# Optimization experiments

Measured on AMD Instinct MI355X. Metric: run time of the kernel, lower is better.

The kernel has to match this reference:

```python
import jax, jax.numpy as jnp
import numpy as np

NEG_INF = -1e9

def setup_inputs() -> dict:
    key = jax.random.key(0)
    ks = jax.random.split(key, 7)
    B, NQ, NK, DQ, DK, DV, DH = 16, 128, 2048, 256, 256, 128, 64
    queries = jax.random.normal(ks[0], (B, NQ, DQ), dtype=jnp.float32)
    keys = jax.random.normal(ks[1], (B, NK, DK), dtype=jnp.float32)
    values = jax.random.normal(ks[2], (B, NK, DV), dtype=jnp.float32)
    valid_lens = jax.random.randint(ks[3], (B,), 1, NK + 1, dtype=jnp.int32)
    Wq = jax.random.normal(ks[4], (DQ, DH), dtype=jnp.float32) / np.sqrt(DQ)
    Wk = jax.random.normal(ks[5], (DK, DH), dtype=jnp.float32) / np.sqrt(DK)
    wv = jax.random.normal(ks[6], (DH,), dtype=jnp.float32) / np.sqrt(DH)
    return {"queries": queries, "keys": keys, "values": values,
            "valid_lens": valid_lens, "Wq": Wq, "Wk": Wk, "wv": wv}


def reference(queries, keys, values, valid_lens, Wq, Wk, wv):
    # Additive (Bahdanau) attention.
    q = jnp.einsum('bqd,dh->bqh', queries, Wq)   # [B, nq, dH]
    k = jnp.einsum('bkd,dh->bkh', keys, Wk)      # [B, nk, dH]
    # broadcast add -> tanh -> reduce with wv: scores [B, nq, nk]
    feat = jnp.tanh(q[:, :, None, :] + k[:, None, :, :])  # [B, nq, nk, dH]
    scores = jnp.einsum('bqkh,h->bqk', feat, wv)
    # masked softmax over nk using per-batch valid lengths
    nk = keys.shape[1]
    mask = jnp.arange(nk)[None, None, :] < valid_lens[:, None, None]  # [B,1,nk]
    scores = jnp.where(mask, scores, NEG_INF)
    attn = jax.nn.softmax(scores, axis=-1)
    # dropout is identity at eval time
    return jnp.einsum('bqk,bkv->bqv', attn, values)  # [B, nq, dv]
```

## Files before the change

kernel.cpp:

```cpp
#include <hip/hip_runtime.h>
#include <stddef.h>


__device__ __forceinline__ float fast_rcp(float x)  { return __builtin_amdgcn_rcpf(x); }
__device__ __forceinline__ float fast_exp2(float x) { return __builtin_amdgcn_exp2f(x); }

#define C2F 2.88539008177792681f
#define L2E 1.44269504088896340f

#if __has_builtin(__builtin_amdgcn_global_load_lds)
#define HAS_GLL 1
__device__ __forceinline__ void gload_lds16(const void* gsrc, void* ldst) {
  __builtin_amdgcn_global_load_lds(
      (const __attribute__((address_space(1))) unsigned int*)gsrc,
      (__attribute__((address_space(3))) unsigned int*)ldst, 16, 0, 0);
}
#else
#define HAS_GLL 0
#endif

#define M_CNTS 0
#define M_NS   1
#define M_PSC  32

template<int MODE>
__device__ __forceinline__
void proj_body(const float* __restrict__ inb, const float* __restrict__ W,
               float* __restrict__ out, const float* __restrict__ wv,
               int b, int r0, int rowsPerB, int t)
{
  __shared__ float4 Wlds[256 * 16];
  __shared__ float  klds[64 * 36];

  const float4* W4 = (const float4*)W;
#if HAS_GLL
  {
    float4* wdst = Wlds + (t & ~63);
    #pragma unroll
    for (int i = 0; i < 16; ++i)
      gload_lds16(W4 + t + 256 * i, wdst + 256 * i);
  }
#else
  #pragma unroll
  for (int i = 0; i < 16; ++i) Wlds[t + 256 * i] = W4[t + 256 * i];
#endif

  const int j = t >> 4;
  const int g = t & 15;

  float acc[4][4];
  #pragma unroll
  for (int m = 0; m < 4; ++m)
    acc[m][0] = acc[m][1] = acc[m][2] = acc[m][3] = 0.f;

  for (int dc = 0; dc < 8; ++dc) {
    {
      const int row = t >> 2, cs = (t & 3) * 8;
      const float* s = inb + row * 256 + dc * 32 + cs;
      float4 a0 = *(const float4*)s;
      float4 a1 = *(const float4*)(s + 4);
      float* dst = &klds[row * 36 + cs];
      *(float4*)dst       = a0;
      *(float4*)(dst + 4) = a1;
    }
    __syncthreads();
    #pragma unroll
    for (int d4 = 0; d4 < 8; ++d4) {
      float4 kv4[4];
      #pragma unroll
      for (int m = 0; m < 4; ++m)
        kv4[m] = *(const float4*)&klds[(g + 16 * m) * 36 + d4 * 4];
      #pragma unroll
      for (int dd = 0; dd < 4; ++dd) {
        float4 w4 = Wlds[(dc * 32 + d4 * 4 + dd) * 16 + j];
        #pragma unroll
        for (int m = 0; m < 4; ++m) {
          float kv = ((const float*)&kv4[m])[dd];
          acc[m][0] = fmaf(kv, w4.x, acc[m][0]);
          acc[m][1] = fmaf(kv, w4.y, acc[m][1]);
          acc[m][2] = fmaf(kv, w4.z, acc[m][2]);
          acc[m][3] = fmaf(kv, w4.w, acc[m][3]);
        }
      }
    }
    __syncthreads();
  }

  if constexpr (MODE == 1) {
    #pragma unroll
    for (int m = 0; m < 4; ++m) {
      int k = r0 + g + 16 * m;
      size_t base = ((size_t)(b * 16 + (k >> 7)) * 64) * 128 + (k & 127);
      #pragma unroll
      for (int i = 0; i < 4; ++i)
        out[base + (size_t)(4 * j + i) * 128] = fast_exp2(C2F * acc[m][i]);
    }
  } else if constexpr (MODE == 2) {
    #pragma unroll
    for (int m = 0; m < 4; ++m) {
      int k = r0 + g + 16 * m;
      size_t base = (size_t)(b * 16 + (k >> 7)) * 8192 + (size_t)(k & 127) * 2;
      float e0 = fast_exp2(C2F * acc[m][0]);
      float e1 = fast_exp2(C2F * acc[m][1]);
      float e2 = fast_exp2(C2F * acc[m][2]);
      float e3 = fast_exp2(C2F * acc[m][3]);
      *(float2*)&out[base + (size_t)(2 * j) * 256]     = make_float2(e0, e1);
      *(float2*)&out[base + (size_t)(2 * j + 1) * 256] = make_float2(e2, e3);
    }
  } else if constexpr (MODE == 3) {
    float4 wq = ((const float4*)wv)[j];
    #pragma unroll
    for (int m = 0; m < 4; ++m) {
      int row = r0 + g + 16 * m;
      float e0 = fast_exp2(C2F * acc[m][0]);
      float e1 = fast_exp2(C2F * acc[m][1]);
      float e2 = fast_exp2(C2F * acc[m][2]);
      float e3 = fast_exp2(C2F * acc[m][3]);
      float4* dst = (float4*)out + ((size_t)(b * 128 + row)) * 32;
      dst[2 * j]     = make_float4(e0, e1, -2.f * wq.x, -2.f * wq.y);
      dst[2 * j + 1] = make_float4(e2, e3, -2.f * wq.z, -2.f * wq.w);
    }
  } else {
    #pragma unroll
    for (int m = 0; m < 4; ++m) {
      int row = r0 + g + 16 * m;
      float4 o;
      o.x = fast_exp2(C2F * acc[m][0]);
      o.y = fast_exp2(C2F * acc[m][1]);
      o.z = fast_exp2(C2F * acc[m][2]);
      o.w = fast_exp2(C2F * acc[m][3]);
      *(float4*)&out[((size_t)b * rowsPerB + row) * 64 + 4 * j] = o;
    }
  }
}

__global__ __launch_bounds__(256)
void proj_qk_kernel(const float* __restrict__ queries, const float* __restrict__ keys,
                    const float* __restrict__ Wq, const float* __restrict__ Wk,
                    float* __restrict__ EqW, float* __restrict__ EkP,
                    const float* __restrict__ wv, const int* __restrict__ vlens,
                    int* __restrict__ meta)
{
  const int blk = blockIdx.x;
  if (blk == 544) {
    if (threadIdx.x == 0) {
      int as = 0;
      meta[M_PSC] = 0;
      for (int b = 0; b < 16; ++b) {
        as += (vlens[b] + 127) >> 7;
        meta[M_PSC + 1 + b] = as;
      }
      meta[M_NS]   = as * 8;
      meta[M_CNTS] = 0;
    }
    return;
  }
  if (blk >= 512) {
    const int idx = blk - 512;
    const int b = idx & 15, rt = idx >> 4, r0 = rt * 64;
    proj_body<3>(queries + ((size_t)b * 128 + r0) * 256, Wq, EqW, wv, b, r0, 128,
                 threadIdx.x);
  } else {
    const int b = blk & 15, rt = blk >> 4, r0 = rt * 64;
    if (r0 >= vlens[b]) return;
    proj_body<2>(keys + ((size_t)b * 2048 + r0) * 256, Wk, EkP, wv, b, r0, 2048,
                 threadIdx.x);
  }
}

template<int MODE, bool CHECK>
__global__ __launch_bounds__(256)
void proj_kernel(const float* __restrict__ in, const float* __restrict__ W,
                 float* __restrict__ out, const int* __restrict__ vlens,
                 int rowsPerB)
{
  const int t  = threadIdx.x;
  const int b  = blockIdx.x & 15;
  const int rt = blockIdx.x >> 4;
  const int r0 = rt * 64;
  if constexpr (CHECK) {
    if (r0 >= vlens[b]) return;
  }
  proj_body<MODE>(in + ((size_t)b * rowsPerB + r0) * 256, W, out,
                  (const float*)nullptr, b, r0, rowsPerB, t);
}

__global__ __launch_bounds__(512, 6)
void scorepv_kernel(const float* __restrict__ EqW, const float* __restrict__ EkP,
                    const float* __restrict__ values, const int* __restrict__ vlens,
                    const float* __restrict__ wv,
                    float* __restrict__ partial, float* __restrict__ tsum,
                    int* __restrict__ meta)
{
  __shared__ float ek_lds[8192];
  __shared__ float eqw_lds[2048];
  __shared__ float p_lds[128 * 20];
  __shared__ int sh_u, sh_pre[17];

  const int t = threadIdx.x;
  if (t < 17) sh_pre[t] = meta[M_PSC + t];
  const int nunits = meta[M_NS];

  float W1 = 0.f, w0 = 0.f;
  #pragma unroll
  for (int u = 0; u < 16; ++u) {
    float4 v = ((const float4*)wv)[u];
    w0 += v.x + v.y + v.z + v.w;
    W1 += fabsf(v.x) + fabsf(v.y) + fabsf(v.z) + fabsf(v.w);
  }

  const int wave_u = __builtin_amdgcn_readfirstlane(t >> 6);
  const int lane   = t & 63;
  const int kp     = lane * 2;
  const int q0l    = wave_u * 2;

  for (;;) {
    __syncthreads();
    if (t == 0) sh_u = atomicAdd(&meta[M_CNTS], 1);
    __syncthreads();
    const int u = sh_u;
    if (u >= nunits) break;

    const int w  = u >> 3;
    const int qq = u & 7;
    int b = 0;
    while (w >= sh_pre[1 + b]) ++b;
    const int kt = w - sh_pre[b];
    const int vl = vlens[b];

    {
      const float4* src  = (const float4*)(EkP + (size_t)(b * 16 + kt) * 8192);
      const float4* qsrc = (const float4*)EqW + ((size_t)(b * 128 + qq * 16)) * 32;
#if HAS_GLL
      float4* dstw = (float4*)ek_lds + (t & ~63);
      #pragma unroll
      for (int i = 0; i < 4; ++i)
        gload_lds16(src + t + 512 * i, dstw + 512 * i);
      gload_lds16(qsrc + t, (float4*)eqw_lds + (t & ~63));
#else
      float4* dst = (float4*)ek_lds;
      #pragma unroll
      for (int i = 0; i < 4; ++i) dst[t + 512 * i] = src[t + 512 * i];
      ((float4*)eqw_lds)[t] = qsrc[t];
#endif
    }
    __syncthreads();

    float s[2][2] = {{w0, w0}, {w0, w0}};
    const float4* ek4 = (const float4*)ek_lds;
    const float4* eqw = (const float4*)eqw_lds;
    #pragma unroll 8
    for (int hp = 0; hp < 32; ++hp) {
      float4 e = ek4[hp * 64 + lane];
      #pragma unroll
      for (int q = 0; q < 2; ++q) {
        float4 ew = eqw[(q0l + q) * 32 + hp];
        { float x0 = fmaf(ew.x, e.x, 1.f), x1 = fmaf(ew.y, e.y, 1.f);
          float y = fast_rcp(x0 * x1);
          float a = ew.w * x0; a = fmaf(ew.z, x1, a);
          s[q][0] = fmaf(a, y, s[q][0]); }
        { float x0 = fmaf(ew.x, e.z, 1.f), x1 = fmaf(ew.y, e.w, 1.f);
          float y = fast_rcp(x0 * x1);
          float a = ew.w * x0; a = fmaf(ew.z, x1, a);
          s[q][1] = fmaf(a, y, s[q][1]); }
      }
    }

    const int kbase = kt * 128 + kp;
    float p[2][2];
    #pragma unroll
    for (int q = 0; q < 2; ++q) {
      p[q][0] = (kbase     < vl) ? fast_exp2((s[q][0] - W1) * L2E) : 0.f;
      p[q][1] = (kbase + 1 < vl) ? fast_exp2((s[q][1] - W1) * L2E) : 0.f;
    }

    *(float2*)&p_lds[kp * 20 + q0l]       = make_float2(p[0][0], p[1][0]);
    *(float2*)&p_lds[(kp + 1) * 20 + q0l] = make_float2(p[0][1], p[1][1]);

    const int q0g = qq * 16 + q0l;
    #pragma unroll
    for (int q = 0; q < 2; ++q) {
      float e = p[q][0] + p[q][1];
      #pragma unroll
      for (int m = 1; m < 64; m <<= 1) e += __shfl_xor(e, m, 64);
      if (lane == 0) tsum[(size_t)(b * 16 + kt) * 128 + q0g + q] = e;
    }
    __syncthreads();

    const int kg = t >> 7, v = t & 127;
    const int kloc = min(128, vl - kt * 128);
    const int k0 = kg * 32, k1 = min(k0 + 32, kloc);
    const int len = (k1 > k0) ? (k1 - k0) : 0;
    const int nfull = len & ~7;
    const float* vb = values + ((size_t)(b * 2048 + kt * 128)) * 128 + v;
    float acc[16];
    #pragma unroll
    for (int i = 0; i < 16; ++i) acc[i] = 0.f;

    for (int kb = k0; kb < k0 + nfull; kb += 8) {
      float vv[8];
      #pragma unroll
      for (int j = 0; j < 8; ++j) vv[j] = vb[(size_t)(kb + j) * 128];
      #pragma unroll
      for (int j = 0; j < 8; ++j) {
        const float* pr = &p_lds[(kb + j) * 20];
        float4 p0 = *(const float4*)&pr[0];
        float4 p1 = *(const float4*)&pr[4];
        float4 p2 = *(const float4*)&pr[8];
        float4 p3 = *(const float4*)&pr[12];
        float vx = vv[j];
        acc[ 0]=fmaf(p0.x,vx,acc[ 0]); acc[ 1]=fmaf(p0.y,vx,acc[ 1]);
        acc[ 2]=fmaf(p0.z,vx,acc[ 2]); acc[ 3]=fmaf(p0.w,vx,acc[ 3]);
        acc[ 4]=fmaf(p1.x,vx,acc[ 4]); acc[ 5]=fmaf(p1.y,vx,acc[ 5]);
        acc[ 6]=fmaf(p1.z,vx,acc[ 6]); acc[ 7]=fmaf(p1.w,vx,acc[ 7]);
        acc[ 8]=fmaf(p2.x,vx,acc[ 8]); acc[ 9]=fmaf(p2.y,vx,acc[ 9]);
        acc[10]=fmaf(p2.z,vx,acc[10]); acc[11]=fmaf(p2.w,vx,acc[11]);
        acc[12]=fmaf(p3.x,vx,acc[12]); acc[13]=fmaf(p3.y,vx,acc[13]);
        acc[14]=fmaf(p3.z,vx,acc[14]); acc[15]=fmaf(p3.w,vx,acc[15]);
      }
    }
    for (int k = k0 + nfull; k < k1; ++k) {
      float vx = vb[(size_t)k * 128];
      const float* pr = &p_lds[k * 20];
      #pragma unroll
      for (int q = 0; q < 16; ++q) acc[q] = fmaf(pr[q], vx, acc[q]);
    }

    __syncthreads();
    float* red = ek_lds;
    if (kg > 0) {
      #pragma unroll
      for (int q = 0; q < 16; ++q) red[(kg - 1) * 2048 + q * 128 + v] = acc[q];
    }
    __syncthreads();
    if (kg == 0) {
      #pragma unroll
      for (int q = 0; q < 16; ++q) {
        float tot = acc[q] + red[q * 128 + v] + red[2048 + q * 128 + v]
                  + red[4096 + q * 128 + v];
        partial[(((size_t)(b * 128 + qq * 16 + q)) * 16 + kt) * 128 + v] = tot;
      }
    }
  }
}

__global__ __launch_bounds__(256)
void reduce_kernel(const float* __restrict__ partial, const float* __restrict__ tsum,
                   const int* __restrict__ vlens, float* __restrict__ out)
{
  const int blk = blockIdx.x;
  const int b   = blk >> 6;
  const int q   = (blk & 63) * 2 + (threadIdx.x >> 7);
  const int v   = threadIdx.x & 127;
  const int ntk = (vlens[b] + 127) >> 7;

  float tot = 0.f;
  for (int i = 0; i < ntk; ++i)
    tot += tsum[(size_t)(b * 16 + i) * 128 + q];

  float acc = 0.f;
  const float* pp = partial + ((size_t)(b * 128 + q)) * 16 * 128 + v;
  for (int i = 0; i < ntk; ++i)
    acc += pp[(size_t)i * 128];

  out[((size_t)(b * 128 + q)) * 128 + v] = acc / tot;
}

__global__ __launch_bounds__(256)
void attn_kernel(const float* __restrict__ Eq, const float* __restrict__ EkT,
                 const float* __restrict__ values, const int* __restrict__ vlens,
                 const float* __restrict__ wv, float* __restrict__ out)
{
  const int t    = threadIdx.x;
  const int b    = blockIdx.x & 15;
  const int qt   = blockIdx.x >> 4;
  const int wave = t >> 6;
  const int lane = t & 63;

  __shared__ float4 sc4[512 * 4];
  __shared__ float  pvp[128 * 5];
  __shared__ float  linvs[4];

  const int vl = vlens[b];

  float eqv[64], wv2[64];
  float w0 = 0.f;
  {
    const float4* eq4 = (const float4*)(Eq + (size_t)(b * 128 + qt * 4 + wave) * 64);
    const float4* wv4 = (const float4*)wv;
    #pragma unroll
    for (int u = 0; u < 16; ++u) {
      float4 e = eq4[u], v = wv4[u];
      eqv[4*u+0] = e.x; eqv[4*u+1] = e.y; eqv[4*u+2] = e.z; eqv[4*u+3] = e.w;
      wv2[4*u+0] = -2.f * v.x; wv2[4*u+1] = -2.f * v.y;
      wv2[4*u+2] = -2.f * v.z; wv2[4*u+3] = -2.f * v.w;
      w0 += v.x + v.y + v.z + v.w;
    }
  }

  const int ktiles = (vl + 127) >> 7;
  const int kp = 2 * lane;
  for (int kt = 0; kt < ktiles; ++kt) {
    const float* tb = EkT + ((size_t)(b * 16 + kt) * 64) * 128 + kp;
    float s0 = w0, s1 = w0;
    #pragma unroll
    for (int h = 0; h < 64; ++h) {
      float2 ek = *(const float2*)(tb + (size_t)h * 128);
      float r0 = fast_rcp(fmaf(eqv[h], ek.x, 1.0f));
      float r1 = fast_rcp(fmaf(eqv[h], ek.y, 1.0f));
      s0 = fmaf(wv2[h], r0, s0);
      s1 = fmaf(wv2[h], r1, s1);
    }
    int k = kt * 128 + kp;
    if (k     >= vl) s0 = -1e9f;
    if (k + 1 >= vl) s1 = -1e9f;
    float* scf = (float*)sc4;
    *(float2*)(scf + (((k >> 2) * 4 + wave) * 4 + (k & 3))) = make_float2(s0, s1);
  }

  const int nq4 = (vl + 3) >> 2;
  float mx = -3e38f;
  for (int Q = lane; Q < nq4; Q += 64) {
    float4 f = sc4[Q * 4 + wave];
    mx = fmaxf(mx, fmaxf(fmaxf(f.x, f.y), fmaxf(f.z, f.w)));
  }
  #pragma unroll
  for (int msk = 1; msk < 64; msk <<= 1) mx = fmaxf(mx, __shfl_xor(mx, msk, 64));
  float lsum = 0.f;
  for (int Q = lane; Q < nq4; Q += 64) {
    float4 f = sc4[Q * 4 + wave];
    f.x = fast_exp2((f.x - mx) * L2E);
    f.y = fast_exp2((f.y - mx) * L2E);
    f.z = fast_exp2((f.z - mx) * L2E);
    f.w = fast_exp2((f.w - mx) * L2E);
    sc4[Q * 4 + wave] = f;
    lsum += f.x + f.y + f.z + f.w;
  }
  #pragma unroll
  for (int msk = 1; msk < 64; msk <<= 1) lsum += __shfl_xor(lsum, msk, 64);
  if (lane == 0) linvs[wave] = fast_rcp(lsum);
  __syncthreads();

  const int grp = t >> 7, v = t & 127;
  float acc[4] = {0.f, 0.f, 0.f, 0.f};
  const float* vb = values + (size_t)b * 2048 * 128 + v;
  for (int Q = grp; Q < nq4; Q += 2) {
    float4 p0 = sc4[Q * 4 + 0], p1 = sc4[Q * 4 + 1];
    float4 p2 = sc4[Q * 4 + 2], p3 = sc4[Q * 4 + 3];
    const float* vk = vb + (size_t)(Q * 4) * 128;
    float x;
    x = vk[0];
    acc[0]=fmaf(p0.x,x,acc[0]); acc[1]=fmaf(p1.x,x,acc[1]);
    acc[2]=fmaf(p2.x,x,acc[2]); acc[3]=fmaf(p3.x,x,acc[3]);
    x = vk[128];
    acc[0]=fmaf(p0.y,x,acc[0]); acc[1]=fmaf(p1.y,x,acc[1]);
    acc[2]=fmaf(p2.y,x,acc[2]); acc[3]=fmaf(p3.y,x,acc[3]);
    x = vk[256];
    acc[0]=fmaf(p0.z,x,acc[0]); acc[1]=fmaf(p1.z,x,acc[1]);
    acc[2]=fmaf(p2.z,x,acc[2]); acc[3]=fmaf(p3.z,x,acc[3]);
    x = vk[384];
    acc[0]=fmaf(p0.w,x,acc[0]); acc[1]=fmaf(p1.w,x,acc[1]);
    acc[2]=fmaf(p2.w,x,acc[2]); acc[3]=fmaf(p3.w,x,acc[3]);
  }
  if (grp == 1) {
    #pragma unroll
    for (int qq = 0; qq < 4; ++qq) pvp[v * 5 + qq] = acc[qq];
  }
  __syncthreads();
  if (grp == 0) {
    #pragma unroll
    for (int qq = 0; qq < 4; ++qq) {
      float tot = acc[qq] + pvp[v * 5 + qq];
      out[((size_t)(b * 128) + qt * 4 + qq) * 128 + v] = tot * linvs[qq];
    }
  }
}

extern "C" void kernel_launch(void* const* d_in, const int* in_sizes, int n_in,
                              void* d_out, int out_size, void* d_ws, size_t ws_size,
                              hipStream_t stream) {
  const float* queries = (const float*)d_in[0];
  const float* keys    = (const float*)d_in[1];
  const float* values  = (const float*)d_in[2];
  const int*   vlens   = (const int*)d_in[3];
  const float* Wq      = (const float*)d_in[4];
  const float* Wk      = (const float*)d_in[5];
  const float* wv      = (const float*)d_in[6];
  float* outp = (float*)d_out;

  float* base    = (float*)d_ws;
  float* EqW     = base;
  float* EkP     = base + 262144;
  float* tsumb   = base + 2359296;
  float* partial = base + 2392064;
  int*   meta    = (int*)(base + 6586368);
  const size_t need = (size_t)6586368 * 4 + 256;

  if (ws_size >= need) {
    hipLaunchKernelGGL(proj_qk_kernel, dim3(545), dim3(256), 0, stream,
                       queries, keys, Wq, Wk, EqW, EkP, wv, vlens, meta);
    hipLaunchKernelGGL(scorepv_kernel, dim3(768), dim3(512), 0, stream,
                       EqW, EkP, values, vlens, wv, partial, tsumb, meta);
    hipLaunchKernelGGL(reduce_kernel, dim3(1024), dim3(256), 0, stream,
                       partial, tsumb, vlens, outp);
  } else {
    hipLaunchKernelGGL((proj_kernel<0, false>), dim3(32), dim3(256), 0, stream,
                       queries, Wq, EqW, (const int*)nullptr, 128);
    hipLaunchKernelGGL((proj_kernel<1, true>), dim3(512), dim3(256), 0, stream,
                       keys, Wk, EkP, vlens, 2048);
    hipLaunchKernelGGL(attn_kernel, dim3(512), dim3(256), 0, stream,
                       EqW, EkP, values, vlens, wv, outp);
  }
}
```

Before: 79.44 us.

## Split P·V work by query groups instead of key groups; vectorize reduce

Each thread group in the P·V stage now accumulates 4 queries over the full 128-key tile, instead of 16 queries over a 32-key slice. This removes the cross-group LDS reduction and its two barriers, and cuts accumulator registers. In exchange, each thread reads 4x more value rows, including rows beyond the valid length that are multiplied by zero. The final reduce kernel uses float4 loads and stores with a smaller grid.

```diff
diff --git a/kernel.cpp b/kernel.cpp
--- a/kernel.cpp
+++ b/kernel.cpp
@@ -287,59 +287,30 @@
     }
     __syncthreads();
 
-    const int kg = t >> 7, v = t & 127;
-    const int kloc = min(128, vl - kt * 128);
-    const int k0 = kg * 32, k1 = min(k0 + 32, kloc);
-    const int len = (k1 > k0) ? (k1 - k0) : 0;
-    const int nfull = len & ~7;
+    const int qg = t >> 7, v = t & 127;
     const float* vb = values + ((size_t)(b * 2048 + kt * 128)) * 128 + v;
-    float acc[16];
-    #pragma unroll
-    for (int i = 0; i < 16; ++i) acc[i] = 0.f;
-
-    for (int kb = k0; kb < k0 + nfull; kb += 8) {
+    float acc[4] = {0.f, 0.f, 0.f, 0.f};
+
+    #pragma unroll 2
+    for (int kb = 0; kb < 128; kb += 8) {
       float vv[8];
       #pragma unroll
       for (int j = 0; j < 8; ++j) vv[j] = vb[(size_t)(kb + j) * 128];
       #pragma unroll
       for (int j = 0; j < 8; ++j) {
-        const float* pr = &p_lds[(kb + j) * 20];
-        float4 p0 = *(const float4*)&pr[0];
-        float4 p1 = *(const float4*)&pr[4];
-        float4 p2 = *(const float4*)&pr[8];
-        float4 p3 = *(const float4*)&pr[12];
+        float4 pq = *(const float4*)&p_lds[(kb + j) * 20 + qg * 4];
         float vx = vv[j];
-        acc[ 0]=fmaf(p0.x,vx,acc[ 0]); acc[ 1]=fmaf(p0.y,vx,acc[ 1]);
-        acc[ 2]=fmaf(p0.z,vx,acc[ 2]); acc[ 3]=fmaf(p0.w,vx,acc[ 3]);
-        acc[ 4]=fmaf(p1.x,vx,acc[ 4]); acc[ 5]=fmaf(p1.y,vx,acc[ 5]);
-        acc[ 6]=fmaf(p1.z,vx,acc[ 6]); acc[ 7]=fmaf(p1.w,vx,acc[ 7]);
-        acc[ 8]=fmaf(p2.x,vx,acc[ 8]); acc[ 9]=fmaf(p2.y,vx,acc[ 9]);
-        acc[10]=fmaf(p2.z,vx,acc[10]); acc[11]=fmaf(p2.w,vx,acc[11]);
-        acc[12]=fmaf(p3.x,vx,acc[12]); acc[13]=fmaf(p3.y,vx,acc[13]);
-        acc[14]=fmaf(p3.z,vx,acc[14]); acc[15]=fmaf(p3.w,vx,acc[15]);
+        acc[0] = fmaf(pq.x, vx, acc[0]);
+        acc[1] = fmaf(pq.y, vx, acc[1]);
+        acc[2] = fmaf(pq.z, vx, acc[2]);
+        acc[3] = fmaf(pq.w, vx, acc[3]);
       }
     }
-    for (int k = k0 + nfull; k < k1; ++k) {
-      float vx = vb[(size_t)k * 128];
-      const float* pr = &p_lds[k * 20];
-      #pragma unroll
-      for (int q = 0; q < 16; ++q) acc[q] = fmaf(pr[q], vx, acc[q]);
-    }
-
-    __syncthreads();
-    float* red = ek_lds;
-    if (kg > 0) {
-      #pragma unroll
-      for (int q = 0; q < 16; ++q) red[(kg - 1) * 2048 + q * 128 + v] = acc[q];
-    }
-    __syncthreads();
-    if (kg == 0) {
-      #pragma unroll
-      for (int q = 0; q < 16; ++q) {
-        float tot = acc[q] + red[q * 128 + v] + red[2048 + q * 128 + v]
-                  + red[4096 + q * 128 + v];
-        partial[(((size_t)(b * 128 + qq * 16 + q)) * 16 + kt) * 128 + v] = tot;
-      }
+
+    #pragma unroll
+    for (int i = 0; i < 4; ++i) {
+      partial[(((size_t)(b * 128 + qq * 16 + qg * 4 + i)) * 16 + kt) * 128 + v]
+          = acc[i];
     }
   }
 }
@@ -348,22 +319,26 @@
 void reduce_kernel(const float* __restrict__ partial, const float* __restrict__ tsum,
                    const int* __restrict__ vlens, float* __restrict__ out)
 {
-  const int blk = blockIdx.x;
-  const int b   = blk >> 6;
-  const int q   = (blk & 63) * 2 + (threadIdx.x >> 7);
-  const int v   = threadIdx.x & 127;
+  const int b   = blockIdx.x >> 4;
+  const int qt  = blockIdx.x & 15;
+  const int ql  = threadIdx.x >> 5;
+  const int v4  = (threadIdx.x & 31) * 4;
+  const int q   = qt * 8 + ql;
   const int ntk = (vlens[b] + 127) >> 7;
 
   float tot = 0.f;
   for (int i = 0; i < ntk; ++i)
     tot += tsum[(size_t)(b * 16 + i) * 128 + q];
 
-  float acc = 0.f;
-  const float* pp = partial + ((size_t)(b * 128 + q)) * 16 * 128 + v;
-  for (int i = 0; i < ntk; ++i)
-    acc += pp[(size_t)i * 128];
-
-  out[((size_t)(b * 128 + q)) * 128 + v] = acc / tot;
+  float ax = 0.f, ay = 0.f, az = 0.f, aw = 0.f;
+  const float4* pp = (const float4*)(partial + ((size_t)(b * 128 + q)) * 2048 + v4);
+  for (int i = 0; i < ntk; ++i) {
+    float4 x = pp[(size_t)i * 32];
+    ax += x.x; ay += x.y; az += x.z; aw += x.w;
+  }
+  const float inv = 1.0f / tot;
+  *(float4*)&out[((size_t)(b * 128 + q)) * 128 + v4] =
+      make_float4(ax * inv, ay * inv, az * inv, aw * inv);
 }
 
 __global__ __launch_bounds__(256)
@@ -501,7 +476,7 @@
                        queries, keys, Wq, Wk, EqW, EkP, wv, vlens, meta);
     hipLaunchKernelGGL(scorepv_kernel, dim3(768), dim3(512), 0, stream,
                        EqW, EkP, values, vlens, wv, partial, tsumb, meta);
-    hipLaunchKernelGGL(reduce_kernel, dim3(1024), dim3(256), 0, stream,
+    hipLaunchKernelGGL(reduce_kernel, dim3(256), dim3(256), 0, stream,
                        partial, tsumb, vlens, outp);
   } else {
     hipLaunchKernelGGL((proj_kernel<0, false>), dim3(32), dim3(256), 0, stream,
```

After: 82.39 us. 3.7% more time.
